# Optimization experiments

Hardware: AMD Instinct MI355X
Metric: run time of the kernel (lower is better)

## Reference

```python
import jax, jax.numpy as jnp
import numpy as np

N, L, C_IN, DEM = 64, 2048, 256, 10


def setup_inputs() -> dict:
    key = jax.random.key(0)
    k1, k2, k3, k4 = jax.random.split(key, 4)
    timesteps = jax.random.normal(k1, (N, L, C_IN), dtype=jnp.float32)
    dem = jax.random.normal(k2, (N, DEM), dtype=jnp.float32)
    W1 = jax.random.normal(k3, (DEM, 40), dtype=jnp.float32) * 0.1
    b1 = jnp.zeros((40,), dtype=jnp.float32)
    W2 = jax.random.normal(k4, (40, 20), dtype=jnp.float32) * 0.1
    b2 = jnp.zeros((20,), dtype=jnp.float32)
    return {"timesteps": timesteps, "dem": dem, "W1": W1, "b1": b1, "W2": W2, "b2": b2}


def reference(timesteps, dem, W1, b1, W2, b2):
    # dem MLP: Linear(10,40) -> ReLU -> (Dropout p=0, eval) -> Linear(40,20) -> ReLU
    h = jax.nn.relu(dem @ W1 + b1)
    dem_emb = jax.nn.relu(h @ W2 + b2)                     # (N, 20)
    n, l, _ = timesteps.shape
    dem_b = jnp.broadcast_to(dem_emb[:, None, :], (n, l, dem_emb.shape[-1]))
    x = jnp.concatenate([timesteps, dem_b], axis=-1)       # (N, L, C)
    # Causal nonzero-average pool: avg_pool1d with kernel=L over (L-1)-left-padded
    # sequence == at step t, sum(x[:t+1]) / count_nonzero(x[:t+1]) per channel.
    csum = jnp.cumsum(x, axis=1)                           # (N, L, C)
    ccnt = jnp.cumsum((x != 0).astype(x.dtype), axis=1)    # (N, L, C)
    p_avg = csum / jnp.maximum(ccnt, 1.0)
    return jax.nn.relu(p_avg)
```

## Files before the change

kernel.cpp:

```cpp
#include <hip/hip_runtime.h>


#define NB 64
#define LL 2048
#define CIN 256
#define COUT 276
#define DEMD 10
#define H1 40
#define H2 20
#define SEG 32
#define LSEG (LL / SEG)
#define UB 8
#define NBATCH (LSEG / UB)

__global__ __launch_bounds__(256) void pme_partials(
    const float* __restrict__ ts,
    float* __restrict__ part)
{
    const int tid  = threadIdx.x;
    const int w    = tid >> 6;
    const int lane = tid & 63;

    const int unit = blockIdx.x * 4 + w;
    const int seg  = unit & (SEG - 1);
    const int n    = unit >> 5;

    const float4* tp = (const float4*)(ts + ((size_t)n * LL + seg * LSEG) * CIN) + lane;

    float4 sum = make_float4(0.f, 0.f, 0.f, 0.f);
    float4 cnt = make_float4(0.f, 0.f, 0.f, 0.f);

    float4 v[2][UB];
#pragma unroll
    for (int u = 0; u < UB; ++u)
        v[0][u] = tp[(size_t)u * (CIN / 4)];

    for (int bb = 0; bb < NBATCH; ++bb) {
        const int cur = bb & 1;
        if (bb + 1 < NBATCH) {
#pragma unroll
            for (int u = 0; u < UB; ++u)
                v[cur ^ 1][u] = tp[(size_t)((bb + 1) * UB + u) * (CIN / 4)];
        }
#pragma unroll
        for (int u = 0; u < UB; ++u) {
            float4 x = v[cur][u];
            sum.x += x.x; cnt.x += (x.x != 0.f) ? 1.f : 0.f;
            sum.y += x.y; cnt.y += (x.y != 0.f) ? 1.f : 0.f;
            sum.z += x.z; cnt.z += (x.z != 0.f) ? 1.f : 0.f;
            sum.w += x.w; cnt.w += (x.w != 0.f) ? 1.f : 0.f;
        }
    }

    float4* pp = (float4*)(part + (((size_t)n * SEG + seg) * 256 + lane * 4) * 2);
    pp[0] = make_float4(sum.x, cnt.x, sum.y, cnt.y);
    pp[1] = make_float4(sum.z, cnt.z, sum.w, cnt.w);
}

__global__ __launch_bounds__(256) void pme_scan(
    const float* __restrict__ ts,
    const float* __restrict__ part,
    const float* __restrict__ dem,
    const float* __restrict__ W1, const float* __restrict__ b1,
    const float* __restrict__ W2, const float* __restrict__ b2,
    float* __restrict__ out)
{
    const int tid  = threadIdx.x;
    const int w    = tid >> 6;
    const int lane = tid & 63;

    const int unit = blockIdx.x * 4 + w;
    const int seg  = unit & (SEG - 1);
    const int n    = unit >> 5;

    const float* dn = dem + n * DEMD;
    float h[H1];
#pragma unroll
    for (int k = 0; k < H1; ++k) {
        float hk = b1[k];
#pragma unroll
        for (int i = 0; i < DEMD; ++i)
            hk += dn[i] * W1[i * H1 + k];
        h[k] = fmaxf(hk, 0.f);
    }
    float4 e4q = make_float4(0.f, 0.f, 0.f, 0.f);
    {
        const int q = (lane < 5) ? lane : 0;
        float e0 = b2[q * 4 + 0], e1 = b2[q * 4 + 1], e2 = b2[q * 4 + 2], e3 = b2[q * 4 + 3];
#pragma unroll
        for (int k = 0; k < H1; ++k) {
            e0 += h[k] * W2[k * H2 + q * 4 + 0];
            e1 += h[k] * W2[k * H2 + q * 4 + 1];
            e2 += h[k] * W2[k * H2 + q * 4 + 2];
            e3 += h[k] * W2[k * H2 + q * 4 + 3];
        }
        e4q = make_float4(fmaxf(e0, 0.f), fmaxf(e1, 0.f), fmaxf(e2, 0.f), fmaxf(e3, 0.f));
    }

    float4 acc = make_float4(0.f, 0.f, 0.f, 0.f);
    float4 cnt = make_float4(0.f, 0.f, 0.f, 0.f);
    const float4* pp = (const float4*)part + (size_t)n * SEG * 128 + lane * 2;
    for (int s = 0; s < seg; ++s) {
        float4 a  = pp[(size_t)s * 128];
        float4 bq = pp[(size_t)s * 128 + 1];
        acc.x += a.x;  cnt.x += a.y;
        acc.y += a.z;  cnt.y += a.w;
        acc.z += bq.x; cnt.z += bq.y;
        acc.w += bq.z; cnt.w += bq.w;
    }

    const float4* tp = (const float4*)(ts + ((size_t)n * LL + seg * LSEG) * CIN) + lane;
    float* oprow = out + ((size_t)n * LL + seg * LSEG) * COUT;

    float4 v[2][UB];
#pragma unroll
    for (int u = 0; u < UB; ++u)
        v[0][u] = tp[(size_t)u * (CIN / 4)];

    for (int bb = 0; bb < NBATCH; ++bb) {
        const int cur = bb & 1;
        if (bb + 1 < NBATCH) {
#pragma unroll
            for (int u = 0; u < UB; ++u)
                v[cur ^ 1][u] = tp[(size_t)((bb + 1) * UB + u) * (CIN / 4)];
        }
#pragma unroll
        for (int u = 0; u < UB; ++u) {
            float4 x = v[cur][u];
            float4 r;
            acc.x += x.x; cnt.x += (x.x != 0.f) ? 1.f : 0.f;
            acc.y += x.y; cnt.y += (x.y != 0.f) ? 1.f : 0.f;
            acc.z += x.z; cnt.z += (x.z != 0.f) ? 1.f : 0.f;
            acc.w += x.w; cnt.w += (x.w != 0.f) ? 1.f : 0.f;
            r.x = fmaxf(acc.x * __builtin_amdgcn_rcpf(fmaxf(cnt.x, 1.f)), 0.f);
            r.y = fmaxf(acc.y * __builtin_amdgcn_rcpf(fmaxf(cnt.y, 1.f)), 0.f);
            r.z = fmaxf(acc.z * __builtin_amdgcn_rcpf(fmaxf(cnt.z, 1.f)), 0.f);
            r.w = fmaxf(acc.w * __builtin_amdgcn_rcpf(fmaxf(cnt.w, 1.f)), 0.f);
            float* rowp = oprow + (size_t)(bb * UB + u) * COUT;
            *(float4*)(rowp + lane * 4) = r;
            if (lane < 5)
                *(float4*)(rowp + CIN + lane * 4) = e4q;
        }
    }
}

extern "C" void kernel_launch(void* const* d_in, const int* in_sizes, int n_in,
                              void* d_out, int out_size, void* d_ws, size_t ws_size,
                              hipStream_t stream) {
    const float* ts  = (const float*)d_in[0];
    const float* dem = (const float*)d_in[1];
    const float* W1  = (const float*)d_in[2];
    const float* b1  = (const float*)d_in[3];
    const float* W2  = (const float*)d_in[4];
    const float* b2  = (const float*)d_in[5];
    float* out  = (float*)d_out;
    float* part = (float*)d_ws;

    pme_partials<<<(NB * SEG) / 4, 256, 0, stream>>>(ts, part);
    pme_scan<<<(NB * SEG) / 4, 256, 0, stream>>>(ts, part, dem, W1, b1, W2, b2, out);
}
```

Measured before the change: 337.3 us.

## Double segments, add prefix-scan kernel over partials, use nontemporal output stores

Doubles the number of sequence segments per batch, giving more waves and shorter serial chains in both passes. A new small kernel turns the per-segment partial sums into exclusive prefixes, so each scan wave loads one prefix instead of looping over all earlier segments. Output stores become nontemporal to avoid polluting cache with write-only data. The cost is an extra kernel launch and a serial prefix loop over 64 segments, run by only 16 blocks.

```diff
diff --git a/kernel.cpp b/kernel.cpp
--- a/kernel.cpp
+++ b/kernel.cpp
@@ -8,10 +8,17 @@
 #define DEMD 10
 #define H1 40
 #define H2 20
-#define SEG 32
+#define SEG 64
 #define LSEG (LL / SEG)
 #define UB 8
 #define NBATCH (LSEG / UB)
+
+typedef float vfloat4 __attribute__((ext_vector_type(4)));
+
+static __device__ __forceinline__ void nt_store4(float* p, float4 v) {
+    vfloat4 t = {v.x, v.y, v.z, v.w};
+    __builtin_nontemporal_store(t, (vfloat4*)p);
+}
 
 __global__ __launch_bounds__(256) void pme_partials(
     const float* __restrict__ ts,
@@ -23,7 +30,7 @@
 
     const int unit = blockIdx.x * 4 + w;
     const int seg  = unit & (SEG - 1);
-    const int n    = unit >> 5;
+    const int n    = unit >> 6;
 
     const float4* tp = (const float4*)(ts + ((size_t)n * LL + seg * LSEG) * CIN) + lane;
 
@@ -52,9 +59,31 @@
         }
     }
 
-    float4* pp = (float4*)(part + (((size_t)n * SEG + seg) * 256 + lane * 4) * 2);
+    float4* pp = (float4*)part + ((size_t)n * SEG + seg) * 128 + lane * 2;
     pp[0] = make_float4(sum.x, cnt.x, sum.y, cnt.y);
     pp[1] = make_float4(sum.z, cnt.z, sum.w, cnt.w);
+}
+
+__global__ __launch_bounds__(256) void pme_prefix(
+    float* __restrict__ part)
+{
+    const int tid  = threadIdx.x;
+    const int w    = tid >> 6;
+    const int lane = tid & 63;
+    const int n    = blockIdx.x * 4 + w;
+
+    float4* p = (float4*)part + (size_t)n * SEG * 128 + lane * 2;
+
+    float4 ra = make_float4(0.f, 0.f, 0.f, 0.f);
+    float4 rb = make_float4(0.f, 0.f, 0.f, 0.f);
+    for (int s = 0; s < SEG; ++s) {
+        float4 a = p[(size_t)s * 128];
+        float4 b = p[(size_t)s * 128 + 1];
+        p[(size_t)s * 128]     = ra;
+        p[(size_t)s * 128 + 1] = rb;
+        ra.x += a.x; ra.y += a.y; ra.z += a.z; ra.w += a.w;
+        rb.x += b.x; rb.y += b.y; rb.z += b.z; rb.w += b.w;
+    }
 }
 
 __global__ __launch_bounds__(256) void pme_scan(
@@ -71,7 +100,7 @@
 
     const int unit = blockIdx.x * 4 + w;
     const int seg  = unit & (SEG - 1);
-    const int n    = unit >> 5;
+    const int n    = unit >> 6;
 
     const float* dn = dem + n * DEMD;
     float h[H1];
@@ -97,17 +126,11 @@
         e4q = make_float4(fmaxf(e0, 0.f), fmaxf(e1, 0.f), fmaxf(e2, 0.f), fmaxf(e3, 0.f));
     }
 
-    float4 acc = make_float4(0.f, 0.f, 0.f, 0.f);
-    float4 cnt = make_float4(0.f, 0.f, 0.f, 0.f);
-    const float4* pp = (const float4*)part + (size_t)n * SEG * 128 + lane * 2;
-    for (int s = 0; s < seg; ++s) {
-        float4 a  = pp[(size_t)s * 128];
-        float4 bq = pp[(size_t)s * 128 + 1];
-        acc.x += a.x;  cnt.x += a.y;
-        acc.y += a.z;  cnt.y += a.w;
-        acc.z += bq.x; cnt.z += bq.y;
-        acc.w += bq.z; cnt.w += bq.w;
-    }
+    const float4* pp = (const float4*)part + ((size_t)n * SEG + seg) * 128 + lane * 2;
+    float4 a  = pp[0];
+    float4 bq = pp[1];
+    float4 acc = make_float4(a.x,  a.z,  bq.x, bq.z);
+    float4 cnt = make_float4(a.y,  a.w,  bq.y, bq.w);
 
     const float4* tp = (const float4*)(ts + ((size_t)n * LL + seg * LSEG) * CIN) + lane;
     float* oprow = out + ((size_t)n * LL + seg * LSEG) * COUT;
@@ -137,9 +160,9 @@
             r.z = fmaxf(acc.z * __builtin_amdgcn_rcpf(fmaxf(cnt.z, 1.f)), 0.f);
             r.w = fmaxf(acc.w * __builtin_amdgcn_rcpf(fmaxf(cnt.w, 1.f)), 0.f);
             float* rowp = oprow + (size_t)(bb * UB + u) * COUT;
-            *(float4*)(rowp + lane * 4) = r;
+            nt_store4(rowp + lane * 4, r);
             if (lane < 5)
-                *(float4*)(rowp + CIN + lane * 4) = e4q;
+                nt_store4(rowp + CIN + lane * 4, e4q);
         }
     }
 }
@@ -157,5 +180,6 @@
     float* part = (float*)d_ws;
 
     pme_partials<<<(NB * SEG) / 4, 256, 0, stream>>>(ts, part);
+    pme_prefix<<<NB / 4, 256, 0, stream>>>(part);
     pme_scan<<<(NB * SEG) / 4, 256, 0, stream>>>(ts, part, dem, W1, b1, W2, b2, out);
 }
```

New measurement: 298.4 us. 11.5% less time.
